# Kernel optimization log

Measured on AMD Instinct MI355X. Metric: run time of the kernel, lower is better.

## Reference

```python
import jax, jax.numpy as jnp
import numpy as np

N_NODES = 100000
N_EDGES = 1600000
N_FEAT = 128
N_CLASSES = 64
K_HOPS = 2


def setup_inputs() -> dict:
    key = jax.random.key(0)
    k1, k2, k3 = jax.random.split(key, 3)
    x = jax.random.normal(k1, (N_NODES, N_FEAT), dtype=jnp.float32)
    edge_index = jax.random.randint(k2, (2, N_EDGES), 0, N_NODES, dtype=jnp.int64)
    # Linear layer params (PyG Linear: y = x @ W.T + b)
    lim = 1.0 / np.sqrt(N_FEAT)
    W = jax.random.uniform(k3, (N_CLASSES, N_FEAT), dtype=jnp.float32, minval=-lim, maxval=lim)
    b = jnp.zeros((N_CLASSES,), dtype=jnp.float32)
    return {"x": x, "edge_index": edge_index, "W": W, "b": b}


def _gcn_norm(edge_index, num_nodes):
    # Add self-loops with weight 1 (PyG gcn_norm default)
    loops = jnp.arange(num_nodes, dtype=edge_index.dtype)
    row = jnp.concatenate([edge_index[0], loops])
    col = jnp.concatenate([edge_index[1], loops])
    ew = jnp.ones(row.shape[0], dtype=jnp.float32)
    deg = jax.ops.segment_sum(ew, col, num_segments=num_nodes)
    dinv = jnp.where(deg > 0, jax.lax.rsqrt(deg), 0.0)
    norm = dinv[row] * ew * dinv[col]  # [E + N]
    return row, col, norm


def reference(x, edge_index, W, b):
    n = x.shape[0]
    row, col, norm = _gcn_norm(edge_index, n)
    # K rounds of normalized SpMM: out[col] += norm * x[row]
    for _ in range(K_HOPS):
        x = jax.ops.segment_sum(norm[:, None] * x[row], col, num_segments=n)
    # Final linear
    return x @ W.T + b
```

## Files before the change

### kernel.cpp

```cpp
#include <hip/hip_runtime.h>
#include <hip/hip_fp16.h>

#define NFEAT 128
#define NCLS  64
#define CPB   96
#define SCAP  1800
#define NBMAX 1056
#define PCHUNK 4096

typedef _Float16 f16;
typedef __attribute__((ext_vector_type(8))) _Float16 f16x8;
typedef __attribute__((ext_vector_type(4))) float f32x4;

__global__ __launch_bounds__(256) void fat_k(const float* __restrict__ x,
                                             const float* __restrict__ W,
                                             const int* __restrict__ row,
                                             const int* __restrict__ col, int E,
                                             int* __restrict__ bcursor,
                                             int* __restrict__ ebuf,
                                             f16* __restrict__ u0,
                                             int n, int NB, int PB) {
    __shared__ union {
        struct { int h[NBMAX]; int cur[NBMAX]; } p;
        __align__(16) f16 zbuf[4][16][64];
    } sh;
    int t = threadIdx.x;

    if ((int)blockIdx.x < PB) {
        int start = blockIdx.x * PCHUNK;
        int end   = min(start + PCHUNK, E);
        for (int i = t; i < NB; i += 256) sh.p.h[i] = 0;
        __syncthreads();
        for (int e = start + t; e < end; e += 256)
            atomicAdd(&sh.p.h[col[e] / CPB], 1);
        __syncthreads();
        for (int i = t; i < NB; i += 256)
            sh.p.cur[i] = i * SCAP + (sh.p.h[i] ? atomicAdd(&bcursor[i], sh.p.h[i]) : 0);
        __syncthreads();
        for (int e = start + t; e < end; e += 256) {
            int c = col[e], b = c / CPB, cl = c - b * CPB;
            int pos = atomicAdd(&sh.p.cur[b], 1);
            if (pos < (b + 1) * SCAP)
                ebuf[pos] = row[e] | (cl << 17);
        }
        return;
    }

    int w = t >> 6, l = t & 63;
    int lr = l & 15;
    int lk = l >> 4;

    f16x8 bfrag[4][4];
#pragma unroll
    for (int ct = 0; ct < 4; ++ct)
#pragma unroll
        for (int m = 0; m < 4; ++m) {
            const float* wp = &W[(size_t)(ct * 16 + lr) * NFEAT + m * 32 + lk * 8];
            float4 w0 = *reinterpret_cast<const float4*>(wp);
            float4 w1 = *reinterpret_cast<const float4*>(wp + 4);
            f16x8 bb;
            bb[0] = (f16)w0.x; bb[1] = (f16)w0.y; bb[2] = (f16)w0.z; bb[3] = (f16)w0.w;
            bb[4] = (f16)w1.x; bb[5] = (f16)w1.y; bb[6] = (f16)w1.z; bb[7] = (f16)w1.w;
            bfrag[ct][m] = bb;
        }

    int nb = (blockIdx.x - PB) * 64 + w * 16;
    int arow = nb + lr;
    bool aok = arow < n;
    const float* xp = &x[(size_t)(aok ? arow : 0) * NFEAT + lk * 8];

    f32x4 acc[4];
#pragma unroll
    for (int ct = 0; ct < 4; ++ct) acc[ct] = (f32x4){0.f, 0.f, 0.f, 0.f};

#pragma unroll
    for (int m = 0; m < 4; ++m) {
        float4 x0 = make_float4(0.f, 0.f, 0.f, 0.f);
        float4 x1 = make_float4(0.f, 0.f, 0.f, 0.f);
        if (aok) {
            x0 = *reinterpret_cast<const float4*>(xp + m * 32);
            x1 = *reinterpret_cast<const float4*>(xp + m * 32 + 4);
        }
        f16x8 a;
        a[0] = (f16)x0.x; a[1] = (f16)x0.y; a[2] = (f16)x0.z; a[3] = (f16)x0.w;
        a[4] = (f16)x1.x; a[5] = (f16)x1.y; a[6] = (f16)x1.z; a[7] = (f16)x1.w;
#pragma unroll
        for (int ct = 0; ct < 4; ++ct)
            acc[ct] = __builtin_amdgcn_mfma_f32_16x16x32_f16(a, bfrag[ct][m], acc[ct], 0, 0, 0);
    }

#pragma unroll
    for (int ct = 0; ct < 4; ++ct)
#pragma unroll
        for (int r = 0; r < 4; ++r)
            sh.zbuf[w][lk * 4 + r][ct * 16 + lr] = (f16)acc[ct][r];
    __builtin_amdgcn_s_waitcnt(0);

    const uint4* zb = reinterpret_cast<const uint4*>(&sh.zbuf[w][0][0]);
    uint4 v0 = zb[l * 2], v1 = zb[l * 2 + 1];
    int node = nb + (l >> 2);
    if (node < n) {
        uint4* op = reinterpret_cast<uint4*>(&u0[(size_t)node * NCLS + (l & 3) * 16]);
        op[0] = v0; op[1] = v1;
    }
}

__global__ __launch_bounds__(256) void sort_k(const int* __restrict__ ebuf,
                                              const int* __restrict__ bcursor,
                                              const f16* __restrict__ u0,
                                              f16* __restrict__ z0,
                                              float* __restrict__ dinv,
                                              int2* __restrict__ pc,
                                              int* __restrict__ csr, int N) {
    __shared__ int sld[SCAP];
    __shared__ int h[CPB];
    __shared__ int cur[CPB];
    __shared__ int sc[256];
    __shared__ float ds[CPB];
    int b = blockIdx.x, t = threadIdx.x;
    int base = b * SCAP;
    int cntb = min(bcursor[b], SCAP);
    if (t < CPB) h[t] = 0;
    for (int j = t; j < cntb; j += 256) sld[j] = ebuf[base + j];
    __syncthreads();
    for (int j = t; j < cntb; j += 256)
        atomicAdd(&h[sld[j] >> 17], 1);
    __syncthreads();
    int v = (t < CPB) ? h[t] : 0;
    sc[t] = v;
    for (int off = 1; off < CPB; off <<= 1) {
        __syncthreads();
        int a = (t >= off) ? sc[t - off] : 0;
        __syncthreads();
        sc[t] += a;
    }
    __syncthreads();
    if (t < CPB) {
        int c = b * CPB + t;
        int p = base + sc[t] - v;
        cur[t] = p;
        float d = rsqrtf((float)(v + 1));
        ds[t] = d;
        if (c < N) {
            pc[c] = make_int2(p, v);
            dinv[c] = d;
        }
    }
    __syncthreads();
    for (int j = t; j < cntb; j += 256) {
        int e = sld[j];
        int pos = atomicAdd(&cur[e >> 17], 1);
        csr[pos] = e & 0x1FFFF;
    }
    int nodes = min(CPB, N - b * CPB);
    if (nodes > 0) {
        const uint4* up = reinterpret_cast<const uint4*>(u0 + (size_t)b * CPB * NCLS);
        uint4* zp = reinterpret_cast<uint4*>(z0 + (size_t)b * CPB * NCLS);
        int tot = nodes * 8;
        for (int i = t; i < tot; i += 256) {
            float d = ds[i >> 3];
            uint4 vv = up[i];
            __half2* hv = reinterpret_cast<__half2*>(&vv);
#pragma unroll
            for (int k = 0; k < 4; ++k) {
                float2 f = __half22float2(hv[k]);
                hv[k] = __floats2half2_rn(f.x * d, f.y * d);
            }
            zp[i] = vv;
        }
    }
}

template <int FINAL>
__global__ __launch_bounds__(256) void spmm_k(const __half* __restrict__ zin,
                                              void* __restrict__ outp,
                                              const int2* __restrict__ pc,
                                              const float* __restrict__ dinv,
                                              const int* __restrict__ csr,
                                              const float* __restrict__ bias, int n) {
    int t = threadIdx.x;
    int lane = t & 63;
    int wid  = blockIdx.x * 4 + (t >> 6);
    wid = __builtin_amdgcn_readfirstlane(wid);
    if (wid >= n) return;

    int sub = lane >> 3;
    int cg  = (lane & 7) * 8;

#define GATHER(r) (*reinterpret_cast<const uint4*>(&zin[(size_t)(r) * NCLS + cg]))

    int2 se = pc[wid];
    uint4 sv = GATHER(wid);
    float d = dinv[wid];
    int s = se.x, e = s + se.y;

    float a[8];
#pragma unroll
    for (int k = 0; k < 8; ++k) a[k] = 0.f;

#define ACCUM(u)                                                            \
    {                                                                       \
        __half2 t0 = *reinterpret_cast<const __half2*>(&u.x);               \
        __half2 t1 = *reinterpret_cast<const __half2*>(&u.y);               \
        __half2 t2 = *reinterpret_cast<const __half2*>(&u.z);               \
        __half2 t3 = *reinterpret_cast<const __half2*>(&u.w);               \
        float2 f0 = __half22float2(t0), f1 = __half22float2(t1);            \
        float2 f2 = __half22float2(t2), f3 = __half22float2(t3);            \
        a[0] += f0.x; a[1] += f0.y; a[2] += f1.x; a[3] += f1.y;             \
        a[4] += f2.x; a[5] += f2.y; a[6] += f3.x; a[7] += f3.y;             \
    }

    int j = s;
    while (e - j >= 32) {
        int r0 = csr[j + sub],      r1 = csr[j + 8 + sub];
        int r2 = csr[j + 16 + sub], r3 = csr[j + 24 + sub];
        uint4 g0 = GATHER(r0), g1 = GATHER(r1), g2 = GATHER(r2), g3 = GATHER(r3);
        ACCUM(g0); ACCUM(g1); ACCUM(g2); ACCUM(g3);
        j += 32;
    }
    int f = (e - j) >> 3;
    uint4 g0, g1, g2, g3;
    bool p = (j + f * 8 + sub) < e;
    if (f > 0) { int r = csr[j + sub];           g0 = GATHER(r); }
    if (f > 1) { int r = csr[j + 8 + sub];       g1 = GATHER(r); }
    if (f > 2) { int r = csr[j + 16 + sub];      g2 = GATHER(r); }
    if (p)     { int r = csr[j + f * 8 + sub];   g3 = GATHER(r); }
    if (f > 0) ACCUM(g0);
    if (f > 1) ACCUM(g1);
    if (f > 2) ACCUM(g2);
    if (p)     ACCUM(g3);

#pragma unroll
    for (int m = 8; m <= 32; m <<= 1)
#pragma unroll
        for (int k = 0; k < 8; ++k)
            a[k] += __shfl_xor(a[k], m, 64);

    ACCUM(sv);
#undef GATHER
#undef ACCUM

    if (FINAL) {
        float* out = (float*)outp;
        float4 b0 = *reinterpret_cast<const float4*>(&bias[cg]);
        float4 b1 = *reinterpret_cast<const float4*>(&bias[cg + 4]);
        if (sub == 0) {
            float4 o0, o1;
            o0.x = fmaf(d, a[0], b0.x); o0.y = fmaf(d, a[1], b0.y);
            o0.z = fmaf(d, a[2], b0.z); o0.w = fmaf(d, a[3], b0.w);
            o1.x = fmaf(d, a[4], b1.x); o1.y = fmaf(d, a[5], b1.y);
            o1.z = fmaf(d, a[6], b1.z); o1.w = fmaf(d, a[7], b1.w);
            *reinterpret_cast<float4*>(&out[(size_t)wid * NCLS + cg])     = o0;
            *reinterpret_cast<float4*>(&out[(size_t)wid * NCLS + cg + 4]) = o1;
        }
    } else {
        __half* zo = (__half*)outp;
        float d2 = d * d;
        if (sub == 0) {
            __half2 h0 = __floats2half2_rn(d2 * a[0], d2 * a[1]);
            __half2 h1 = __floats2half2_rn(d2 * a[2], d2 * a[3]);
            __half2 h2 = __floats2half2_rn(d2 * a[4], d2 * a[5]);
            __half2 h3 = __floats2half2_rn(d2 * a[6], d2 * a[7]);
            uint4 pk;
            pk.x = *reinterpret_cast<unsigned int*>(&h0);
            pk.y = *reinterpret_cast<unsigned int*>(&h1);
            pk.z = *reinterpret_cast<unsigned int*>(&h2);
            pk.w = *reinterpret_cast<unsigned int*>(&h3);
            *reinterpret_cast<uint4*>(&zo[(size_t)wid * NCLS + cg]) = pk;
        }
    }
}

extern "C" void kernel_launch(void* const* d_in, const int* in_sizes, int n_in,
                              void* d_out, int out_size, void* d_ws, size_t ws_size,
                              hipStream_t stream) {
    const float* x  = (const float*)d_in[0];
    const int*   ei = (const int*)d_in[1];
    const float* W  = (const float*)d_in[2];
    const float* b  = (const float*)d_in[3];

    const int N = in_sizes[0] / NFEAT;
    const int E = in_sizes[1] / 2;
    const int* row = ei;
    const int* col = ei + E;
    const int NB = (N + CPB - 1) / CPB;
    if (NB > NBMAX) return;

    const int PB    = (E + PCHUNK - 1) / PCHUNK;
    const int PROJB = (N + 63) / 64;

    const size_t SLOTS = (size_t)NB * SCAP;
    f16*   u0      = (f16*)d_ws;
    f16*   z0      = u0 + (size_t)N * NCLS;
    int*   ebuf    = (int*)(z0 + (size_t)N * NCLS);
    int*   csr     = ebuf + SLOTS;
    float* dinv    = (float*)(csr + SLOTS);
    int2*  pc      = (int2*)(dinv + N);
    int*   bcursor = (int*)(pc + N);

    size_t needed = (size_t)N * NCLS * 2 * 2
                  + (SLOTS * 2 + (size_t)N * 3 + (size_t)NB) * 4;
    if (ws_size < needed) return;

    hipMemsetAsync(bcursor, 0, (size_t)NB * 4, stream);
    fat_k<<<PB + PROJB, 256, 0, stream>>>(x, W, row, col, E, bcursor, ebuf, u0, N, NB, PB);
    sort_k<<<NB, 256, 0, stream>>>(ebuf, bcursor, u0, z0, dinv, pc, csr, N);

    f16* z1 = u0;
    spmm_k<0><<<(N + 3) / 4, 256, 0, stream>>>((const __half*)z0, (void*)z1, pc, dinv, csr, b, N);
    spmm_k<1><<<(N + 3) / 4, 256, 0, stream>>>((const __half*)z1, d_out,     pc, dinv, csr, b, N);
}
```

Before: 239.7 us.

## Double bucket size and block width, split sort into degree-scale and scatter kernels

```diff
diff --git a/kernel.cpp b/kernel.cpp
--- a/kernel.cpp
+++ b/kernel.cpp
@@ -3,16 +3,16 @@
 
 #define NFEAT 128
 #define NCLS  64
-#define CPB   96
-#define SCAP  1800
-#define NBMAX 1056
-#define PCHUNK 4096
+#define CPB   192
+#define SCAP  3600
+#define NBMAX 544
+#define PCHUNK 8192
 
 typedef _Float16 f16;
 typedef __attribute__((ext_vector_type(8))) _Float16 f16x8;
 typedef __attribute__((ext_vector_type(4))) float f32x4;
 
-__global__ __launch_bounds__(256) void fat_k(const float* __restrict__ x,
+__global__ __launch_bounds__(512) void fat_k(const float* __restrict__ x,
                                              const float* __restrict__ W,
                                              const int* __restrict__ row,
                                              const int* __restrict__ col, int E,
@@ -22,22 +22,22 @@
                                              int n, int NB, int PB) {
     __shared__ union {
         struct { int h[NBMAX]; int cur[NBMAX]; } p;
-        __align__(16) f16 zbuf[4][16][64];
+        __align__(16) f16 zbuf[8][16][64];
     } sh;
     int t = threadIdx.x;
 
     if ((int)blockIdx.x < PB) {
         int start = blockIdx.x * PCHUNK;
         int end   = min(start + PCHUNK, E);
-        for (int i = t; i < NB; i += 256) sh.p.h[i] = 0;
-        __syncthreads();
-        for (int e = start + t; e < end; e += 256)
+        for (int i = t; i < NB; i += 512) sh.p.h[i] = 0;
+        __syncthreads();
+        for (int e = start + t; e < end; e += 512)
             atomicAdd(&sh.p.h[col[e] / CPB], 1);
         __syncthreads();
-        for (int i = t; i < NB; i += 256)
+        for (int i = t; i < NB; i += 512)
             sh.p.cur[i] = i * SCAP + (sh.p.h[i] ? atomicAdd(&bcursor[i], sh.p.h[i]) : 0);
         __syncthreads();
-        for (int e = start + t; e < end; e += 256) {
+        for (int e = start + t; e < end; e += 512) {
             int c = col[e], b = c / CPB, cl = c - b * CPB;
             int pos = atomicAdd(&sh.p.cur[b], 1);
             if (pos < (b + 1) * SCAP)
@@ -64,7 +64,7 @@
             bfrag[ct][m] = bb;
         }
 
-    int nb = (blockIdx.x - PB) * 64 + w * 16;
+    int nb = (blockIdx.x - PB) * 128 + w * 16;
     int arow = nb + lr;
     bool aok = arow < n;
     const float* xp = &x[(size_t)(aok ? arow : 0) * NFEAT + lk * 8];
@@ -105,59 +105,48 @@
     }
 }
 
-__global__ __launch_bounds__(256) void sort_k(const int* __restrict__ ebuf,
-                                              const int* __restrict__ bcursor,
-                                              const f16* __restrict__ u0,
-                                              f16* __restrict__ z0,
-                                              float* __restrict__ dinv,
-                                              int2* __restrict__ pc,
-                                              int* __restrict__ csr, int N) {
-    __shared__ int sld[SCAP];
+__global__ __launch_bounds__(512) void degscale_k(const int* __restrict__ ebuf,
+                                                  const int* __restrict__ bcursor,
+                                                  const f16* __restrict__ u0,
+                                                  f16* __restrict__ z0,
+                                                  float* __restrict__ dinv,
+                                                  int2* __restrict__ pc, int N) {
     __shared__ int h[CPB];
-    __shared__ int cur[CPB];
     __shared__ int sc[256];
     __shared__ float ds[CPB];
     int b = blockIdx.x, t = threadIdx.x;
+    if (t < CPB) h[t] = 0;
+    __syncthreads();
     int base = b * SCAP;
     int cntb = min(bcursor[b], SCAP);
-    if (t < CPB) h[t] = 0;
-    for (int j = t; j < cntb; j += 256) sld[j] = ebuf[base + j];
-    __syncthreads();
-    for (int j = t; j < cntb; j += 256)
-        atomicAdd(&h[sld[j] >> 17], 1);
+    for (int j = t; j < cntb; j += 512)
+        atomicAdd(&h[ebuf[base + j] >> 17], 1);
     __syncthreads();
     int v = (t < CPB) ? h[t] : 0;
-    sc[t] = v;
-    for (int off = 1; off < CPB; off <<= 1) {
-        __syncthreads();
-        int a = (t >= off) ? sc[t - off] : 0;
-        __syncthreads();
-        sc[t] += a;
+    if (t < 256) sc[t] = v;
+    for (int off = 1; off < 256; off <<= 1) {
+        __syncthreads();
+        int a = (t >= off && t < 256) ? sc[t - off] : 0;
+        __syncthreads();
+        if (t < 256) sc[t] += a;
     }
     __syncthreads();
     if (t < CPB) {
         int c = b * CPB + t;
-        int p = base + sc[t] - v;
-        cur[t] = p;
         float d = rsqrtf((float)(v + 1));
         ds[t] = d;
         if (c < N) {
-            pc[c] = make_int2(p, v);
+            pc[c] = make_int2(base + sc[t] - v, v);
             dinv[c] = d;
         }
     }
     __syncthreads();
-    for (int j = t; j < cntb; j += 256) {
-        int e = sld[j];
-        int pos = atomicAdd(&cur[e >> 17], 1);
-        csr[pos] = e & 0x1FFFF;
-    }
     int nodes = min(CPB, N - b * CPB);
     if (nodes > 0) {
         const uint4* up = reinterpret_cast<const uint4*>(u0 + (size_t)b * CPB * NCLS);
         uint4* zp = reinterpret_cast<uint4*>(z0 + (size_t)b * CPB * NCLS);
         int tot = nodes * 8;
-        for (int i = t; i < tot; i += 256) {
+        for (int i = t; i < tot; i += 512) {
             float d = ds[i >> 3];
             uint4 vv = up[i];
             __half2* hv = reinterpret_cast<__half2*>(&vv);
@@ -168,6 +157,26 @@
             }
             zp[i] = vv;
         }
+    }
+}
+
+__global__ __launch_bounds__(512) void sort_k(const int* __restrict__ ebuf,
+                                              const int* __restrict__ bcursor,
+                                              const int2* __restrict__ pc,
+                                              int* __restrict__ csr, int N) {
+    __shared__ int cur[CPB];
+    int b = blockIdx.x, t = threadIdx.x;
+    if (t < CPB) {
+        int c = b * CPB + t;
+        cur[t] = (c < N) ? pc[c].x : 0;
+    }
+    __syncthreads();
+    int base = b * SCAP;
+    int cntb = min(bcursor[b], SCAP);
+    for (int j = t; j < cntb; j += 512) {
+        int e = ebuf[base + j];
+        int pos = atomicAdd(&cur[e >> 17], 1);
+        csr[pos] = e & 0x1FFFF;
     }
 }
 
@@ -287,7 +296,7 @@
     if (NB > NBMAX) return;
 
     const int PB    = (E + PCHUNK - 1) / PCHUNK;
-    const int PROJB = (N + 63) / 64;
+    const int PROJB = (N + 127) / 128;
 
     const size_t SLOTS = (size_t)NB * SCAP;
     f16*   u0      = (f16*)d_ws;
@@ -303,8 +312,9 @@
     if (ws_size < needed) return;
 
     hipMemsetAsync(bcursor, 0, (size_t)NB * 4, stream);
-    fat_k<<<PB + PROJB, 256, 0, stream>>>(x, W, row, col, E, bcursor, ebuf, u0, N, NB, PB);
-    sort_k<<<NB, 256, 0, stream>>>(ebuf, bcursor, u0, z0, dinv, pc, csr, N);
+    fat_k<<<PB + PROJB, 512, 0, stream>>>(x, W, row, col, E, bcursor, ebuf, u0, N, NB, PB);
+    degscale_k<<<NB, 512, 0, stream>>>(ebuf, bcursor, u0, z0, dinv, pc, N);
+    sort_k<<<NB, 512, 0, stream>>>(ebuf, bcursor, pc, csr, N);
 
     f16* z1 = u0;
     spmm_k<0><<<(N + 3) / 4, 256, 0, stream>>>((const __half*)z0, (void*)z1, pc, dinv, csr, b, N);
```

New measurement: 238.8 us. No clear change (-0.4%).
